# Kernel tuning notes

Measured on AMD Instinct MI355X. Metric: run time of the kernel, lower is better.

## Reference

```python
import jax, jax.numpy as jnp
import numpy as np

T, B, D, H = 512, 64, 1024, 1024  # seq_len, batch, input_dim, hidden (out_dim, bi_dir=False)


def setup_inputs() -> dict:
    key = jax.random.key(0)
    k = jax.random.split(key, 5)
    s = 1.0 / np.sqrt(H)  # PyTorch LSTMCell init scale
    x = jax.random.normal(k[0], (T, B, D), dtype=jnp.float32)
    W_ih = jax.random.uniform(k[1], (4 * H, D), minval=-s, maxval=s, dtype=jnp.float32)
    W_hh = jax.random.uniform(k[2], (4 * H, H), minval=-s, maxval=s, dtype=jnp.float32)
    b_ih = jax.random.uniform(k[3], (4 * H,), minval=-s, maxval=s, dtype=jnp.float32)
    b_hh = jax.random.uniform(k[4], (4 * H,), minval=-s, maxval=s, dtype=jnp.float32)
    return {"x": x, "W_ih": W_ih, "W_hh": W_hh, "b_ih": b_ih, "b_hh": b_hh}


def reference(x, W_ih, W_hh, b_ih, b_hh):
    # Unidirectional LSTM over [T, B, D] -> [T, B, H], PyTorch LSTMCell gate order i,f,g,o.
    # Precompute input contribution for all timesteps in one big GEMM.
    xg = jnp.einsum('tbd,gd->tbg', x, W_ih) + b_ih + b_hh  # [T, B, 4H]

    def step(carry, xg_t):
        h, c = carry
        gates = xg_t + h @ W_hh.T  # [B, 4H]
        i, f, g, o = jnp.split(gates, 4, axis=-1)
        c = jax.nn.sigmoid(f) * c + jax.nn.sigmoid(i) * jnp.tanh(g)
        h = jax.nn.sigmoid(o) * jnp.tanh(c)
        return (h, c), h

    h0 = jnp.zeros((B, H), dtype=x.dtype)
    c0 = jnp.zeros((B, H), dtype=x.dtype)
    _, hs = jax.lax.scan(step, (h0, c0), xg)  # hs: [T, B, H]
    return hs
```

## Files before the change

kernel.cpp:

```cpp
#include <hip/hip_runtime.h>
#include <hip/hip_bf16.h>
#include <stdint.h>

#define T_STEPS 512
#define BATCH   64
#define DIM     1024
#define HID     1024
#define NG      4096
#define MROWS   (T_STEPS * BATCH)

typedef __bf16 bf16;
typedef __bf16 bf16x4 __attribute__((ext_vector_type(4)));
typedef __bf16 bf16x8 __attribute__((ext_vector_type(8)));
typedef float  f32x4  __attribute__((ext_vector_type(4)));
typedef unsigned int u32;
typedef u32 u32x2 __attribute__((ext_vector_type(2)));
typedef u32 u32x4 __attribute__((ext_vector_type(4)));

__device__ __forceinline__ void g2lds16(const void* g, void* l) {
    __builtin_amdgcn_global_load_lds(
        (const __attribute__((address_space(1))) void*)g,
        (__attribute__((address_space(3))) void*)l, 16, 0, 0);
}

__device__ __forceinline__ float fsigmoid(float x) {
    return 1.0f / (1.0f + __expf(-x));
}
__device__ __forceinline__ float ftanh_(float x) {
    return 1.0f - 2.0f / (__expf(2.0f * x) + 1.0f);
}

__device__ __forceinline__ u32x4 load16_cc(const void* p) {
    u32x4 r;
    asm volatile("global_load_dwordx4 %0, %1, off sc0 sc1" : "=v"(r) : "v"(p) : "memory");
    return r;
}
__device__ __forceinline__ void store2_cc(void* p, u32 v) {
    asm volatile("global_store_short %0, %1, off sc0 sc1" :: "v"(p), "v"(v) : "memory");
}
__device__ __forceinline__ u32x2 load8_cached(const void* p) {
    u32x2 r;
    asm volatile("global_load_dwordx2 %0, %1, off" : "=v"(r) : "v"(p) : "memory");
    return r;
}
__device__ __forceinline__ void store4_f32(float* p, float v) {
    asm volatile("global_store_dword %0, %1, off" :: "v"(p), "v"(v) : "memory");
}
#define WAITVM(n) asm volatile("s_waitcnt vmcnt(" #n ")" ::: "memory")

__global__ __launch_bounds__(256) void prep_kernel(
    const float* __restrict__ x,   const float* __restrict__ wih,
    const float* __restrict__ whh, const float* __restrict__ bih,
    const float* __restrict__ bhh,
    bf16* __restrict__ xb, bf16* __restrict__ wihp, bf16* __restrict__ wfrag,
    float* __restrict__ bsump, bf16* __restrict__ hbuf, u32* __restrict__ flags)
{
    const int nt  = gridDim.x * blockDim.x;
    const int gid = blockIdx.x * blockDim.x + threadIdx.x;

    for (int i = gid; i < MROWS * DIM / 4; i += nt) {
        f32x4 v = *(const f32x4*)(x + (size_t)i * 4);
        bf16x4 o = {(bf16)v[0], (bf16)v[1], (bf16)v[2], (bf16)v[3]};
        *(bf16x4*)(xb + (size_t)i * 4) = o;
    }
    for (int i = gid; i < NG * (DIM / 4); i += nt) {
        const int n = i >> 8, c4 = (i & 255) * 4;
        f32x4 v = *(const f32x4*)(wih + (size_t)n * DIM + c4);
        bf16x4 o = {(bf16)v[0], (bf16)v[1], (bf16)v[2], (bf16)v[3]};
        const int np = ((n & 1023) << 2) | (n >> 10);
        *(bf16x4*)(wihp + (size_t)np * DIM + c4) = o;
    }
    for (int i = gid; i < NG * HID / 8; i += nt) {
        const int lane = i & 63;
        const int f    = (i >> 6) & 63;
        const int wv   = (i >> 12) & 3;
        const int hg   = i >> 14;
        const int n = f & 7, kk = f >> 3;
        const int grow = (lane & 3) * 1024 + hg * 32 + n * 4 + ((lane & 15) >> 2);
        const int k0   = wv * 256 + kk * 32 + (lane >> 4) * 8;
        f32x4 v0 = *(const f32x4*)(whh + (size_t)grow * HID + k0);
        f32x4 v1 = *(const f32x4*)(whh + (size_t)grow * HID + k0 + 4);
        bf16x8 o = {(bf16)v0[0], (bf16)v0[1], (bf16)v0[2], (bf16)v0[3],
                    (bf16)v1[0], (bf16)v1[1], (bf16)v1[2], (bf16)v1[3]};
        *(bf16x8*)(wfrag + (size_t)i * 8) = o;
    }
    for (int i = gid; i < NG; i += nt)
        bsump[((i & 1023) << 2) | (i >> 10)] = bih[i] + bhh[i];
    for (int i = gid; i < BATCH * HID / 4; i += nt) {
        bf16x4 z = {(bf16)0.f, (bf16)0.f, (bf16)0.f, (bf16)0.f};
        *(bf16x4*)(hbuf + (size_t)i * 4) = z;
    }
    for (int i = gid; i < 256 * 16; i += nt)
        flags[i] = 0u;
}

__global__ __launch_bounds__(256) void gemm_kernel(
    const bf16* __restrict__ A, const bf16* __restrict__ B,
    const float* __restrict__ bsum, bf16* __restrict__ xgp)
{
    __shared__ char lds[16384];
    char* As = lds;
    char* Bs = lds + 8192;

    const int tid  = threadIdx.x;
    const int lane = tid & 63;
    const int wv   = tid >> 6;
    const int wr   = wv >> 1, wc = wv & 1;
    const int bx   = blockIdx.x & 31;
    const int by   = blockIdx.x >> 5;
    const int m0   = by * 128, n0 = bx * 128;

    f32x4 acc[4][4] = {};

    const int r4 = tid >> 2;
    const int c8 = (tid & 3) * 8;
    const size_t arow0 = (size_t)(m0 +      r4) * DIM + c8;
    const size_t arow1 = (size_t)(m0 + 64 + r4) * DIM + c8;
    const size_t brow0 = (size_t)(n0 +      r4) * DIM + c8;
    const size_t brow1 = (size_t)(n0 + 64 + r4) * DIM + c8;
    const int ldsoff = tid * 16;

    for (int k0 = 0; k0 < DIM; k0 += 32) {
        g2lds16(A + arow0 + k0, As + ldsoff);
        g2lds16(A + arow1 + k0, As + 4096 + ldsoff);
        g2lds16(B + brow0 + k0, Bs + ldsoff);
        g2lds16(B + brow1 + k0, Bs + 4096 + ldsoff);
        __syncthreads();

        bf16x8 af[4], bfr[4];
        #pragma unroll
        for (int i = 0; i < 4; ++i) {
            af[i]  = *(const bf16x8*)(As + (wr*64 + i*16 + (lane & 15))*64 + (lane >> 4)*16);
            bfr[i] = *(const bf16x8*)(Bs + (wc*64 + i*16 + (lane & 15))*64 + (lane >> 4)*16);
        }
        #pragma unroll
        for (int i = 0; i < 4; ++i)
            #pragma unroll
            for (int j = 0; j < 4; ++j)
                acc[i][j] = __builtin_amdgcn_mfma_f32_16x16x32_bf16(
                    af[i], bfr[j], acc[i][j], 0, 0, 0);
        __syncthreads();
    }

    #pragma unroll
    for (int j = 0; j < 4; ++j) {
        const int nn = n0 + wc*64 + j*16 + (lane & 15);
        const float bias = bsum[nn];
        #pragma unroll
        for (int i = 0; i < 4; ++i) {
            #pragma unroll
            for (int r = 0; r < 4; ++r) {
                const int mm = m0 + wr*64 + i*16 + ((lane >> 4) << 2) + r;
                xgp[(size_t)mm * NG + nn] = (bf16)(acc[i][j][r] + bias);
            }
        }
    }
}

__global__ __launch_bounds__(256, 1) void lstm_kernel(
    const bf16* __restrict__ xgp, const bf16* __restrict__ wfrag,
    bf16* __restrict__ hbuf, u32* __restrict__ flags, float* __restrict__ out)
{
    __shared__ char  hstage[8 * 2064];
    __shared__ float gbuf[4][8][136];

    const int tid  = threadIdx.x;
    const int lane = tid & 63;
    const int wv   = tid >> 6;
    const int wg   = blockIdx.x;
    const int hg   = wg & 31;
    const int bg   = wg >> 5;

    bf16x8 wreg[64];
    {
        const bf16* wb = wfrag + ((size_t)(hg * 4 + wv) * 4096 + lane) * 8;
        #pragma unroll
        for (int f = 0; f < 64; ++f)
            wreg[f] = *(const bf16x8*)(wb + (size_t)f * 512);
    }

    const int frow  = lane & 15;
    const int b_el  = tid >> 5;
    const int j_el  = tid & 31;
    const int hid   = hg * 32 + j_el;

    const int goff = (lane >> 3) * 2048 + wv * 512 + (lane & 7) * 16;
    const int woff = (lane >> 3) * 2064 + wv * 512 + (lane & 7) * 16;
    const int rbase = frow & 7;
    const int cbase = rbase * 2064 + wv * 512 + (lane >> 4) * 16;

    const u32* pollpA = flags + ((bg * 32 + wv * 8 + (lane & 3)) << 4);
    const u32* pollpB = flags + ((bg * 32 + wv * 8 + 4 + (lane & 3)) << 4);
    u32* myflag       = flags + ((bg * 32 + hg) << 4);

    float c = 0.f;
    u32x2 xr = load8_cached(xgp + (size_t)(bg * 8 + b_el) * NG + hid * 4);

    #pragma unroll 1
    for (int step = 0; step < T_STEPS; ++step) {
        while (__hip_atomic_load(pollpA, __ATOMIC_RELAXED,
                                 __HIP_MEMORY_SCOPE_AGENT) < (u32)step)
            __builtin_amdgcn_s_sleep(1);

        const char* hbp = (const char*)(hbuf + (step & 1) * (BATCH * HID)
                                             + (size_t)(bg * 8) * HID);
        u32x4 s0 = load16_cc(hbp + goff);
        u32x4 s1 = load16_cc(hbp + goff + 128);

        while (__hip_atomic_load(pollpB, __ATOMIC_RELAXED,
                                 __HIP_MEMORY_SCOPE_AGENT) < (u32)step)
            __builtin_amdgcn_s_sleep(1);

        u32x4 s2 = load16_cc(hbp + goff + 256);
        u32x4 s3 = load16_cc(hbp + goff + 384);

        *(u32x4*)(hstage + woff)       = s0;
        *(u32x4*)(hstage + woff + 128) = s1;
        f32x4 acc[8] = {};
        #pragma unroll
        for (int kk = 0; kk < 4; ++kk) {
            bf16x8 a = *(const bf16x8*)(hstage + cbase + kk * 64);
            #pragma unroll
            for (int n = 0; n < 8; ++n)
                acc[n] = __builtin_amdgcn_mfma_f32_16x16x32_bf16(
                    a, wreg[kk * 8 + n], acc[n], 0, 0, 0);
        }

        WAITVM(0);
        __builtin_amdgcn_sched_barrier(0);
        *(u32x4*)(hstage + woff + 256) = s2;
        *(u32x4*)(hstage + woff + 384) = s3;
        #pragma unroll
        for (int kk = 4; kk < 8; ++kk) {
            bf16x8 a = *(const bf16x8*)(hstage + cbase + kk * 64);
            #pragma unroll
            for (int n = 0; n < 8; ++n)
                acc[n] = __builtin_amdgcn_mfma_f32_16x16x32_bf16(
                    a, wreg[kk * 8 + n], acc[n], 0, 0, 0);
        }

        if (lane < 32) {
            const int q = lane >> 4;
            #pragma unroll
            for (int n = 0; n < 8; ++n)
                #pragma unroll
                for (int r = 0; r < 4; ++r)
                    gbuf[wv][q * 4 + r][n * 16 + frow] = acc[n][r];
        }
        __syncthreads();

        bf16x4 xv = __builtin_bit_cast(bf16x4, xr);
        float P[4];
        #pragma unroll
        for (int g = 0; g < 4; ++g)
            P[g] = gbuf[0][b_el][j_el * 4 + g] + gbuf[1][b_el][j_el * 4 + g]
                 + gbuf[2][b_el][j_el * 4 + g] + gbuf[3][b_el][j_el * 4 + g]
                 + (float)xv[g];
        const float ig = fsigmoid(P[0]);
        const float fg = fsigmoid(P[1]);
        const float gg = ftanh_(P[2]);
        const float og = fsigmoid(P[3]);
        c = fg * c + ig * gg;
        const float hv = og * ftanh_(c);

        const bf16 h16 = (bf16)hv;
        store2_cc(hbuf + ((step & 1) ^ 1) * (BATCH * HID)
                       + (size_t)(bg * 8 + b_el) * HID + hid,
                  (u32)__builtin_bit_cast(unsigned short, h16));
        store4_f32(out + (size_t)(step * BATCH + bg * 8 + b_el) * HID + hid, hv);
        const int nx = (step + 1 < T_STEPS) ? step + 1 : step;
        xr = load8_cached(xgp + ((size_t)(nx * BATCH) + bg * 8 + b_el) * NG
                              + hid * 4);
        WAITVM(2);
        __builtin_amdgcn_sched_barrier(0);
        __syncthreads();
        if (tid == 0)
            __hip_atomic_store(myflag, (u32)(step + 1),
                               __ATOMIC_RELAXED, __HIP_MEMORY_SCOPE_AGENT);
    }
}

extern "C" void kernel_launch(void* const* d_in, const int* in_sizes, int n_in,
                              void* d_out, int out_size, void* d_ws, size_t ws_size,
                              hipStream_t stream) {
    const float* x   = (const float*)d_in[0];
    const float* wih = (const float*)d_in[1];
    const float* whh = (const float*)d_in[2];
    const float* bih = (const float*)d_in[3];
    const float* bhh = (const float*)d_in[4];
    float* out = (float*)d_out;

    char* ws = (char*)d_ws;
    size_t off = 0;
    bf16* xgp   = (bf16*)(ws + off); off += (size_t)MROWS * NG * 2;
    bf16* xb    = (bf16*)(ws + off); off += (size_t)MROWS * DIM * 2;
    bf16* wihp  = (bf16*)(ws + off); off += (size_t)NG * DIM * 2;
    bf16* wfrag = (bf16*)(ws + off); off += (size_t)NG * HID * 2;
    float* bsum = (float*)(ws + off); off += (size_t)NG * 4;
    bf16* hbuf  = (bf16*)(ws + off); off += (size_t)2 * BATCH * HID * 2;
    u32* flags  = (u32*)(ws + off); off += 256 * 16 * 4;
    (void)ws_size; (void)in_sizes; (void)n_in; (void)out_size;

    prep_kernel<<<2048, 256, 0, stream>>>(x, wih, whh, bih, bhh,
                                          xb, wihp, wfrag, bsum, hbuf, flags);
    gemm_kernel<<<8192, 256, 0, stream>>>(xb, wihp, bsum, xgp);
    lstm_kernel<<<256, 256, 0, stream>>>(xgp, wfrag, hbuf, flags, out);
}
```

Baseline: 1.896 ms.

## Fuse input GEMM and LSTM recurrence into one kernel with per-row readiness flags

Merges the input-projection GEMM and the recurrent LSTM kernel into a single 512-block launch. 256 blocks compute GEMM tiles in timestep order and bump per-row-block counters, while the other 256 blocks run the recurrence and spin until the xg rows they need are ready. The aim is to overlap the large GEMM with the serial recurrence instead of running them back to back. In exchange it relies on all 512 blocks being co-resident (launch bounds of 2 per CU), adds polling overhead to every step, and has GEMM blocks compete for CU resources with the latency-bound recurrence.

```diff
diff --git a/kernel.cpp b/kernel.cpp
--- a/kernel.cpp
+++ b/kernel.cpp
@@ -35,13 +35,13 @@
     asm volatile("global_load_dwordx4 %0, %1, off sc0 sc1" : "=v"(r) : "v"(p) : "memory");
     return r;
 }
+__device__ __forceinline__ u32x2 load8_cc(const void* p) {
+    u32x2 r;
+    asm volatile("global_load_dwordx2 %0, %1, off sc0 sc1" : "=v"(r) : "v"(p) : "memory");
+    return r;
+}
 __device__ __forceinline__ void store2_cc(void* p, u32 v) {
     asm volatile("global_store_short %0, %1, off sc0 sc1" :: "v"(p), "v"(v) : "memory");
-}
-__device__ __forceinline__ u32x2 load8_cached(const void* p) {
-    u32x2 r;
-    asm volatile("global_load_dwordx2 %0, %1, off" : "=v"(r) : "v"(p) : "memory");
-    return r;
 }
 __device__ __forceinline__ void store4_f32(float* p, float v) {
     asm volatile("global_store_dword %0, %1, off" :: "v"(p), "v"(v) : "memory");
@@ -53,7 +53,8 @@
     const float* __restrict__ whh, const float* __restrict__ bih,
     const float* __restrict__ bhh,
     bf16* __restrict__ xb, bf16* __restrict__ wihp, bf16* __restrict__ wfrag,
-    float* __restrict__ bsump, bf16* __restrict__ hbuf, u32* __restrict__ flags)
+    float* __restrict__ bsump, bf16* __restrict__ hbuf, u32* __restrict__ flags,
+    u32* __restrict__ mrowdone)
 {
     const int nt  = gridDim.x * blockDim.x;
     const int gid = blockIdx.x * blockDim.x + threadIdx.x;
@@ -92,84 +93,91 @@
     }
     for (int i = gid; i < 256 * 16; i += nt)
         flags[i] = 0u;
-}
-
-__global__ __launch_bounds__(256) void gemm_kernel(
-    const bf16* __restrict__ A, const bf16* __restrict__ B,
-    const float* __restrict__ bsum, bf16* __restrict__ xgp)
+    for (int i = gid; i < 256; i += nt)
+        mrowdone[i] = 0u;
+}
+
+__global__ __launch_bounds__(256, 2) void fused_kernel(
+    const bf16* __restrict__ xb, const bf16* __restrict__ wihp,
+    const float* __restrict__ bsum, bf16* __restrict__ xgp,
+    const bf16* __restrict__ wfrag, bf16* __restrict__ hbuf,
+    u32* __restrict__ flags, u32* __restrict__ mrowdone,
+    float* __restrict__ out)
 {
-    __shared__ char lds[16384];
-    char* As = lds;
-    char* Bs = lds + 8192;
-
+    __shared__ __align__(16) char smem[33920];
     const int tid  = threadIdx.x;
     const int lane = tid & 63;
     const int wv   = tid >> 6;
-    const int wr   = wv >> 1, wc = wv & 1;
-    const int bx   = blockIdx.x & 31;
-    const int by   = blockIdx.x >> 5;
-    const int m0   = by * 128, n0 = bx * 128;
-
-    f32x4 acc[4][4] = {};
-
-    const int r4 = tid >> 2;
-    const int c8 = (tid & 3) * 8;
-    const size_t arow0 = (size_t)(m0 +      r4) * DIM + c8;
-    const size_t arow1 = (size_t)(m0 + 64 + r4) * DIM + c8;
-    const size_t brow0 = (size_t)(n0 +      r4) * DIM + c8;
-    const size_t brow1 = (size_t)(n0 + 64 + r4) * DIM + c8;
-    const int ldsoff = tid * 16;
-
-    for (int k0 = 0; k0 < DIM; k0 += 32) {
-        g2lds16(A + arow0 + k0, As + ldsoff);
-        g2lds16(A + arow1 + k0, As + 4096 + ldsoff);
-        g2lds16(B + brow0 + k0, Bs + ldsoff);
-        g2lds16(B + brow1 + k0, Bs + 4096 + ldsoff);
-        __syncthreads();
-
-        bf16x8 af[4], bfr[4];
-        #pragma unroll
-        for (int i = 0; i < 4; ++i) {
-            af[i]  = *(const bf16x8*)(As + (wr*64 + i*16 + (lane & 15))*64 + (lane >> 4)*16);
-            bfr[i] = *(const bf16x8*)(Bs + (wc*64 + i*16 + (lane & 15))*64 + (lane >> 4)*16);
-        }
-        #pragma unroll
-        for (int i = 0; i < 4; ++i)
+
+    if (blockIdx.x < 256) {
+        char* As = smem;
+        char* Bs = smem + 8192;
+        const int wr = wv >> 1, wc = wv & 1;
+        const int r4 = tid >> 2;
+        const int c8 = (tid & 3) * 8;
+        const int ldsoff = tid * 16;
+
+        for (int tno = 0; tno < 32; ++tno) {
+            const int g  = (int)blockIdx.x + tno * 256;
+            const int bx = g & 31, by = g >> 5;
+            const int m0 = by * 128, n0 = bx * 128;
+            const size_t arow0 = (size_t)(m0 +      r4) * DIM + c8;
+            const size_t arow1 = (size_t)(m0 + 64 + r4) * DIM + c8;
+            const size_t brow0 = (size_t)(n0 +      r4) * DIM + c8;
+            const size_t brow1 = (size_t)(n0 + 64 + r4) * DIM + c8;
+
+            f32x4 acc[4][4] = {};
+            for (int k0 = 0; k0 < DIM; k0 += 32) {
+                g2lds16(xb   + arow0 + k0, As + ldsoff);
+                g2lds16(xb   + arow1 + k0, As + 4096 + ldsoff);
+                g2lds16(wihp + brow0 + k0, Bs + ldsoff);
+                g2lds16(wihp + brow1 + k0, Bs + 4096 + ldsoff);
+                __syncthreads();
+
+                bf16x8 af[4], bfr[4];
+                #pragma unroll
+                for (int i = 0; i < 4; ++i) {
+                    af[i]  = *(const bf16x8*)(As + (wr*64 + i*16 + (lane & 15))*64 + (lane >> 4)*16);
+                    bfr[i] = *(const bf16x8*)(Bs + (wc*64 + i*16 + (lane & 15))*64 + (lane >> 4)*16);
+                }
+                #pragma unroll
+                for (int i = 0; i < 4; ++i)
+                    #pragma unroll
+                    for (int j = 0; j < 4; ++j)
+                        acc[i][j] = __builtin_amdgcn_mfma_f32_16x16x32_bf16(
+                            af[i], bfr[j], acc[i][j], 0, 0, 0);
+                __syncthreads();
+            }
+
             #pragma unroll
-            for (int j = 0; j < 4; ++j)
-                acc[i][j] = __builtin_amdgcn_mfma_f32_16x16x32_bf16(
-                    af[i], bfr[j], acc[i][j], 0, 0, 0);
-        __syncthreads();
-    }
-
-    #pragma unroll
-    for (int j = 0; j < 4; ++j) {
-        const int nn = n0 + wc*64 + j*16 + (lane & 15);
-        const float bias = bsum[nn];
-        #pragma unroll
-        for (int i = 0; i < 4; ++i) {
-            #pragma unroll
-            for (int r = 0; r < 4; ++r) {
-                const int mm = m0 + wr*64 + i*16 + ((lane >> 4) << 2) + r;
-                xgp[(size_t)mm * NG + nn] = (bf16)(acc[i][j][r] + bias);
+            for (int j = 0; j < 4; ++j) {
+                const int nn = n0 + wc*64 + j*16 + (lane & 15);
+                const float bias = bsum[nn];
+                #pragma unroll
+                for (int i = 0; i < 4; ++i) {
+                    #pragma unroll
+                    for (int r = 0; r < 4; ++r) {
+                        const int mm = m0 + wr*64 + i*16 + ((lane >> 4) << 2) + r;
+                        const bf16 o16 = (bf16)(acc[i][j][r] + bias);
+                        store2_cc(xgp + (size_t)mm * NG + nn,
+                                  (u32)__builtin_bit_cast(unsigned short, o16));
+                    }
+                }
             }
-        }
-    }
-}
-
-__global__ __launch_bounds__(256, 1) void lstm_kernel(
-    const bf16* __restrict__ xgp, const bf16* __restrict__ wfrag,
-    bf16* __restrict__ hbuf, u32* __restrict__ flags, float* __restrict__ out)
-{
-    __shared__ char  hstage[8 * 2064];
-    __shared__ float gbuf[4][8][136];
-
-    const int tid  = threadIdx.x;
-    const int lane = tid & 63;
-    const int wv   = tid >> 6;
-    const int wg   = blockIdx.x;
-    const int hg   = wg & 31;
-    const int bg   = wg >> 5;
+            WAITVM(0);
+            __syncthreads();
+            if (tid == 0)
+                atomicAdd(&mrowdone[by], 1u);
+        }
+        return;
+    }
+
+    char* hstage = smem;
+    float (*gbuf)[8][136] = reinterpret_cast<float(*)[8][136]>(smem + 16512);
+
+    const int wg = (int)blockIdx.x - 256;
+    const int hg = wg & 31;
+    const int bg = wg >> 5;
 
     bf16x8 wreg[64];
     {
@@ -194,13 +202,24 @@
     u32* myflag       = flags + ((bg * 32 + hg) << 4);
 
     float c = 0.f;
-    u32x2 xr = load8_cached(xgp + (size_t)(bg * 8 + b_el) * NG + hid * 4);
+
+    while (__hip_atomic_load(&mrowdone[0], __ATOMIC_RELAXED,
+                             __HIP_MEMORY_SCOPE_AGENT) < 32u)
+        __builtin_amdgcn_s_sleep(8);
+    u32x2 xr = load8_cc(xgp + (size_t)(bg * 8 + b_el) * NG + hid * 4);
 
     #pragma unroll 1
     for (int step = 0; step < T_STEPS; ++step) {
-        while (__hip_atomic_load(pollpA, __ATOMIC_RELAXED,
-                                 __HIP_MEMORY_SCOPE_AGENT) < (u32)step)
+        const int nx  = (step + 1 < T_STEPS) ? step + 1 : step;
+        const u32* xrdy = mrowdone + (nx >> 1);
+        for (;;) {
+            u32 f = __hip_atomic_load(pollpA, __ATOMIC_RELAXED,
+                                      __HIP_MEMORY_SCOPE_AGENT);
+            u32 gr = __hip_atomic_load(xrdy, __ATOMIC_RELAXED,
+                                       __HIP_MEMORY_SCOPE_AGENT);
+            if (__all((int)(f >= (u32)step && gr >= 32u))) break;
             __builtin_amdgcn_s_sleep(1);
+        }
 
         const char* hbp = (const char*)(hbuf + (step & 1) * (BATCH * HID)
                                              + (size_t)(bg * 8) * HID);
@@ -268,9 +287,8 @@
                        + (size_t)(bg * 8 + b_el) * HID + hid,
                   (u32)__builtin_bit_cast(unsigned short, h16));
         store4_f32(out + (size_t)(step * BATCH + bg * 8 + b_el) * HID + hid, hv);
-        const int nx = (step + 1 < T_STEPS) ? step + 1 : step;
-        xr = load8_cached(xgp + ((size_t)(nx * BATCH) + bg * 8 + b_el) * NG
-                              + hid * 4);
+        xr = load8_cc(xgp + ((size_t)(nx * BATCH) + bg * 8 + b_el) * NG
+                          + hid * 4);
         WAITVM(2);
         __builtin_amdgcn_sched_barrier(0);
         __syncthreads();
@@ -299,10 +317,12 @@
     float* bsum = (float*)(ws + off); off += (size_t)NG * 4;
     bf16* hbuf  = (bf16*)(ws + off); off += (size_t)2 * BATCH * HID * 2;
     u32* flags  = (u32*)(ws + off); off += 256 * 16 * 4;
+    u32* mrowdone = (u32*)(ws + off); off += 256 * 4;
     (void)ws_size; (void)in_sizes; (void)n_in; (void)out_size;
 
     prep_kernel<<<2048, 256, 0, stream>>>(x, wih, whh, bih, bhh,
-                                          xb, wihp, wfrag, bsum, hbuf, flags);
-    gemm_kernel<<<8192, 256, 0, stream>>>(xb, wihp, bsum, xgp);
-    lstm_kernel<<<256, 256, 0, stream>>>(xgp, wfrag, hbuf, flags, out);
-}
+                                          xb, wihp, wfrag, bsum, hbuf, flags,
+                                          mrowdone);
+    fused_kernel<<<512, 256, 0, stream>>>(xb, wihp, bsum, xgp, wfrag,
+                                          hbuf, flags, mrowdone, out);
+}
```

Result: slower. 3.249 ms (+71.4%).
